# Performance work log

Hardware: AMD Instinct MI355X
Metric: run time of the kernel (lower is better)

## Reference

```python
import jax, jax.numpy as jnp
import numpy as np

B, S, D, H, FF = 2, 2048, 1024, 16, 4096
DH = D // H
EPS = 1e-5


def _linear_params(key, din, dout):
    kw, kb = jax.random.split(key)
    lim = 1.0 / np.sqrt(din)
    W = jax.random.uniform(kw, (din, dout), jnp.float32, -lim, lim)
    b = jax.random.uniform(kb, (dout,), jnp.float32, -lim, lim)
    return W, b


def setup_inputs() -> dict:
    key = jax.random.key(0)
    ks = jax.random.split(key, 8)
    x = jax.random.normal(ks[0], (B, S, D), jnp.float32)
    mask = jnp.ones((B, 1, 1, S), jnp.int32)
    wq, bq = _linear_params(ks[1], D, D)
    wk, bk = _linear_params(ks[2], D, D)
    wv, bv = _linear_params(ks[3], D, D)
    w1, b1 = _linear_params(ks[4], D, D)       # linear1 (attn output proj)
    fw1, fb1 = _linear_params(ks[5], D, FF)    # ffn.w_1
    fw2, fb2 = _linear_params(ks[6], FF, D)    # ffn.w_2
    g1 = jnp.ones((D,), jnp.float32); be1 = jnp.zeros((D,), jnp.float32)
    g2 = jnp.ones((D,), jnp.float32); be2 = jnp.zeros((D,), jnp.float32)
    return dict(x=x, mask=mask, wq=wq, bq=bq, wk=wk, bk=bk, wv=wv, bv=bv,
                w1=w1, b1=b1, g1=g1, be1=be1,
                fw1=fw1, fb1=fb1, fw2=fw2, fb2=fb2, g2=g2, be2=be2)


def _layernorm(x, g, b):
    mu = jnp.mean(x, axis=-1, keepdims=True)
    var = jnp.mean(jnp.square(x - mu), axis=-1, keepdims=True)
    return (x - mu) * jax.lax.rsqrt(var + EPS) * g + b


def _encoder(x, mask, wq, bq, wk, bk, wv, bv, w1, b1, g1, be1,
             fw1, fb1, fw2, fb2, g2, be2):
    res = x
    # QKV projections, reshape to [B, H, S, DH]
    q = (x @ wq + bq).reshape(B, S, H, DH).transpose(0, 2, 1, 3)
    k = (x @ wk + bk).reshape(B, S, H, DH).transpose(0, 2, 1, 3)
    v = (x @ wv + bv).reshape(B, S, H, DH).transpose(0, 2, 1, 3)
    scores = jnp.einsum('bhqd,bhkd->bhqk', q, k) / np.sqrt(DH).astype(np.float32)
    scores = jnp.where(mask == 0, jnp.float32(-1e9), scores)
    probs = jax.nn.softmax(scores, axis=-1)  # dropout = identity in eval
    attn = jnp.einsum('bhqk,bhkd->bhqd', probs, v)
    attn = attn.transpose(0, 2, 1, 3).reshape(B, S, D)
    x = _layernorm(attn @ w1 + b1 + res, g1, be1)
    res = x
    ff = jax.nn.relu(x @ fw1 + fb1) @ fw2 + fb2
    return _layernorm(ff + res, g2, be2)


def reference(x, mask, wq, bq, wk, bk, wv, bv, w1, b1, g1, be1,
              fw1, fb1, fw2, fb2, g2, be2):
    return _encoder(x, mask, wq, bq, wk, bk, wv, bv, w1, b1, g1, be1,
                    fw1, fb1, fw2, fb2, g2, be2)
```

## Files before the change

kernel.cpp:

```cpp
#include <hip/hip_runtime.h>
#include <hip/hip_bf16.h>
#include <cstdint>

typedef unsigned short u16;
typedef __attribute__((ext_vector_type(8))) short bf16x8;
typedef __attribute__((ext_vector_type(4))) float f32x4;

#define DEVFN static __device__ __forceinline__

static constexpr int S    = 2048;
static constexpr int D    = 1024;
static constexpr int DHd  = 64;
static constexpr int FFd  = 4096;
static constexpr int M    = 4096;
static constexpr int LDQK = 2048;

static constexpr float SC2 = 0.18033688f;

DEVFN u16 f2b(float v) {
    union { __hip_bfloat16 h; u16 u; } x;
    x.h = __float2bfloat16(v);
    return x.u;
}
DEVFN float b2f(u16 u) {
    union { float f; uint32_t i; } x;
    x.i = ((uint32_t)u) << 16;
    return x.f;
}

typedef const uint32_t __attribute__((address_space(1)))* gptr_t;
typedef uint32_t __attribute__((address_space(3)))* lptr_t;
DEVFN void load16(const void* g, void* l) {
    __builtin_amdgcn_global_load_lds((gptr_t)g, (lptr_t)l, 16, 0, 0);
}

template<int MODE, int KS>
__global__ __launch_bounds__(512, 2)
void gemm256(const u16* __restrict__ A, const u16* __restrict__ BT,
             const float* __restrict__ bias, void* __restrict__ outp,
             u16* __restrict__ vout, int N)
{
    __shared__ __align__(16) u16 Lds[65536];
    const int tid  = threadIdx.x;
    const int lane = tid & 63;
    const int w    = tid >> 6;
    const int wm = w >> 2, wn = w & 3;
    const int g = lane >> 4, c = lane & 15;
    const int c7 = c & 7;
    const int bn0 = blockIdx.x * 256;
    const int bm0 = blockIdx.y * 256;
    const int z   = (MODE == 4) ? (int)blockIdx.z : 0;
    const size_t kofs = (size_t)z * 1024;

    const int sr = tid >> 3;
    const int gl = (tid & 7) ^ (sr & 7);
    const u16* Asrc = A  + (size_t)(bm0 + sr) * KS + kofs + gl * 8;
    const u16* Bsrc = BT + (size_t)(bn0 + sr) * KS + kofs + gl * 8;
    char* dA = (char*)Lds + (size_t)tid * 16;
    char* dB = dA + 32768;

#define STG_A(BUF, H, KT)                                                       \
    { _Pragma("unroll") for (int Lh = 0; Lh < 2; ++Lh)                          \
        load16(Asrc + (size_t)((H)*128 + Lh*64) * KS + (KT)*64,                 \
               dA + (BUF)*65536 + (H)*16384 + Lh*8192); }
#define STG_B(BUF, H, KT)                                                       \
    { _Pragma("unroll") for (int Lh = 0; Lh < 2; ++Lh)                          \
        load16(Bsrc + (size_t)((H)*128 + Lh*64) * KS + (KT)*64,                 \
               dB + (BUF)*65536 + (H)*16384 + Lh*8192); }
#define VMCNT(N_) asm volatile("s_waitcnt vmcnt(" #N_ ")" ::: "memory")
#define BAR() { __builtin_amdgcn_s_barrier(); __builtin_amdgcn_sched_barrier(0); }

    const char* lbase = (const char*)Lds;
    auto rdA = [&](int buf, int i, int kk) -> bf16x8 {
        const int half = i >> 2;
        const int lr = (2*(i & 3) + wm) * 16 + c;
        return *(const bf16x8*)(lbase + buf*65536 + half*16384 + lr*128
                                + (((kk<<2) + g) ^ c7) * 16);
    };
    auto rdB = [&](int buf, int j, int kk) -> bf16x8 {
        const int half = j >> 1;
        const int lr = (j & 1)*64 + wn*16 + c;
        return *(const bf16x8*)(lbase + buf*65536 + 32768 + half*16384 + lr*128
                                + (((kk<<2) + g) ^ c7) * 16);
    };

    const f32x4 fz = {0.f, 0.f, 0.f, 0.f};
    f32x4 acc[8][4];
#pragma unroll
    for (int i = 0; i < 8; ++i)
#pragma unroll
        for (int j = 0; j < 4; ++j) acc[i][j] = fz;

    bf16x8 af[4][2], bf[4][2];

    auto body = [&](int cur, int nxt, int kt, bool stage) {
        if (stage) STG_A(nxt, 0, kt + 1);
#pragma unroll
        for (int i = 0; i < 4; ++i)
#pragma unroll
            for (int kk = 0; kk < 2; ++kk) af[i][kk] = rdA(cur, i, kk);
#pragma unroll
        for (int j = 0; j < 2; ++j)
#pragma unroll
            for (int kk = 0; kk < 2; ++kk) bf[j][kk] = rdB(cur, j, kk);
        __builtin_amdgcn_s_setprio(1);
#pragma unroll
        for (int i = 0; i < 4; ++i)
#pragma unroll
            for (int j = 0; j < 2; ++j)
#pragma unroll
                for (int kk = 0; kk < 2; ++kk)
                    acc[i][j] = __builtin_amdgcn_mfma_f32_16x16x32_bf16(
                        af[i][kk], bf[j][kk], acc[i][j], 0, 0, 0);
        __builtin_amdgcn_s_setprio(0);
        if (stage) { VMCNT(4); } else { VMCNT(2); }
        BAR();
        if (stage) STG_B(nxt, 0, kt + 1);
#pragma unroll
        for (int j = 2; j < 4; ++j)
#pragma unroll
            for (int kk = 0; kk < 2; ++kk) bf[j][kk] = rdB(cur, j, kk);
        __builtin_amdgcn_s_setprio(1);
#pragma unroll
        for (int i = 0; i < 4; ++i)
#pragma unroll
            for (int j = 2; j < 4; ++j)
#pragma unroll
                for (int kk = 0; kk < 2; ++kk)
                    acc[i][j] = __builtin_amdgcn_mfma_f32_16x16x32_bf16(
                        af[i][kk], bf[j][kk], acc[i][j], 0, 0, 0);
        __builtin_amdgcn_s_setprio(0);
        if (stage) { VMCNT(4); } else { VMCNT(0); }
        BAR();
        if (stage) STG_B(nxt, 1, kt + 1);
#pragma unroll
        for (int i = 4; i < 8; ++i)
#pragma unroll
            for (int kk = 0; kk < 2; ++kk) af[i - 4][kk] = rdA(cur, i, kk);
        __builtin_amdgcn_s_setprio(1);
#pragma unroll
        for (int i = 4; i < 8; ++i)
#pragma unroll
            for (int j = 0; j < 2; ++j)
#pragma unroll
                for (int kk = 0; kk < 2; ++kk)
                    acc[i][j] = __builtin_amdgcn_mfma_f32_16x16x32_bf16(
                        af[i - 4][kk], bf[j][kk], acc[i][j], 0, 0, 0);
        __builtin_amdgcn_s_setprio(0);
        if (stage) STG_A(nxt, 1, kt + 1);
        __builtin_amdgcn_s_setprio(1);
#pragma unroll
        for (int i = 4; i < 8; ++i)
#pragma unroll
            for (int j = 2; j < 4; ++j)
#pragma unroll
                for (int kk = 0; kk < 2; ++kk)
                    acc[i][j] = __builtin_amdgcn_mfma_f32_16x16x32_bf16(
                        af[i - 4][kk], bf[j][kk], acc[i][j], 0, 0, 0);
        __builtin_amdgcn_s_setprio(0);
        if (stage) { VMCNT(4); BAR(); }
    };

    STG_A(0, 0, 0); STG_B(0, 0, 0); STG_B(0, 1, 0); STG_A(0, 1, 0);
    VMCNT(4);
    BAR();

#pragma unroll 1
    for (int kt = 0; kt < 14; kt += 2) {
        body(0, 1, kt, true);
        body(1, 0, kt + 1, true);
    }
    body(0, 1, 14, true);
    body(1, 0, 15, false);
#undef STG_A
#undef STG_B
#undef VMCNT
#undef BAR

#pragma unroll
    for (int i = 0; i < 8; ++i) {
        const int fm = (i >> 2) * 8 + (i & 3) * 2 + wm;
        const int row = bm0 + fm * 16 + 4 * g;
#pragma unroll
        for (int j = 0; j < 4; ++j) {
            const int fn = (j >> 1) * 8 + (j & 1) * 4 + wn;
            const int col = bn0 + fn * 16 + c;
            if (MODE == 4) {
                u16* outz = (u16*)outp + (size_t)z * M * D;
#pragma unroll
                for (int r = 0; r < 4; ++r)
                    outz[(size_t)(row + r) * D + col] = f2b(acc[i][j][r]);
            } else if (MODE == 3 && col >= 2048) {
                const float bv = bias[col];
                union { u16 u[4]; uint2 v; } pk;
#pragma unroll
                for (int r = 0; r < 4; ++r) pk.u[r] = f2b(acc[i][j][r] + bv);
                const size_t vidx = ((size_t)(row >> 11) * 1024 + (col - 2048))
                                    * (size_t)S + (row & 2047);
                *(uint2*)&vout[vidx] = pk.v;
            } else {
                const float bv = bias[col];
                const float sc = (MODE == 3 && col < D) ? SC2 : 1.f;
                const int nn = (MODE == 3) ? LDQK : N;
#pragma unroll
                for (int r = 0; r < 4; ++r) {
                    float v = acc[i][j][r] + bv;
                    if (MODE == 2) v = v > 0.f ? v : 0.f;
                    v *= sc;
                    ((u16*)outp)[(size_t)(row + r) * nn + col] = f2b(v);
                }
            }
        }
    }
}

template<int KTOT>
__global__ __launch_bounds__(256, 3)
void gemm_splitk(const u16* __restrict__ A, const u16* __restrict__ BT,
                 u16* __restrict__ part)
{
    __shared__ __align__(16) u16 As[128 * 64];
    __shared__ __align__(16) u16 Bs[128 * 64];
    const int tid  = threadIdx.x;
    const int lane = tid & 63;
    const int w    = tid >> 6;
    const int wm = w >> 1, wn = w & 1;
    const int g = lane >> 4, c = lane & 15;
    const int bn0 = blockIdx.x * 128;
    const int bm0 = blockIdx.y * 128;
    const int z   = blockIdx.z;
    const int srow = tid >> 3;
    const int scol = (tid & 7) * 8;

    const f32x4 fz = {0.f, 0.f, 0.f, 0.f};
    f32x4 acc[4][4];
#pragma unroll
    for (int i = 0; i < 4; ++i)
#pragma unroll
        for (int j = 0; j < 4; ++j) acc[i][j] = fz;

    const u16* Ab = A  + (size_t)(bm0 + srow) * KTOT + z * (KTOT/2) + scol;
    const u16* Bb = BT + (size_t)(bn0 + srow) * KTOT + z * (KTOT/2) + scol;
    char* AsB = (char*)As + (size_t)tid * 16;
    char* BsB = (char*)Bs + (size_t)tid * 16;

    for (int kt = 0; kt < KTOT/128; ++kt) {
        const int k0 = kt << 6;
        __syncthreads();
#pragma unroll
        for (int cc = 0; cc < 4; ++cc) {
            load16(Ab + (size_t)(cc * 32) * KTOT + k0, AsB + cc * 4096);
            load16(Bb + (size_t)(cc * 32) * KTOT + k0, BsB + cc * 4096);
        }
        __syncthreads();
#pragma unroll
        for (int kk = 0; kk < 2; ++kk) {
            bf16x8 af[4], bfv[4];
#pragma unroll
            for (int i = 0; i < 4; ++i)
                af[i] = *(const bf16x8*)&As[(wm*64 + i*16 + c) * 64 + kk*32 + g*8];
#pragma unroll
            for (int j = 0; j < 4; ++j)
                bfv[j] = *(const bf16x8*)&Bs[(wn*64 + j*16 + c) * 64 + kk*32 + g*8];
#pragma unroll
            for (int i = 0; i < 4; ++i)
#pragma unroll
                for (int j = 0; j < 4; ++j)
                    acc[i][j] = __builtin_amdgcn_mfma_f32_16x16x32_bf16(
                        af[i], bfv[j], acc[i][j], 0, 0, 0);
        }
    }

    u16* outz = part + (size_t)z * M * D;
#pragma unroll
    for (int i = 0; i < 4; ++i) {
        const int row = bm0 + wm*64 + i*16 + g*4;
#pragma unroll
        for (int j = 0; j < 4; ++j) {
            const int col = bn0 + wn*64 + j*16 + c;
#pragma unroll
            for (int r = 0; r < 4; ++r)
                outz[(size_t)(row + r) * D + col] = f2b(acc[i][j][r]);
        }
    }
}

template<int NPART>
__global__ __launch_bounds__(256)
void ln_part_fused(const u16* __restrict__ part, const float* __restrict__ bias,
                   const float* __restrict__ resid, const float* __restrict__ gam,
                   const float* __restrict__ bet, u16* __restrict__ out_b,
                   float* __restrict__ out_f)
{
    const int row = blockIdx.x;
    const int tid = threadIdx.x;
    __shared__ float red1[4], red2[4];
    const float4 bv = ((const float4*)bias)[tid];
    const float4 rv = ((const float4*)(resid + (size_t)row * D))[tid];
    float y0 = bv.x + rv.x, y1 = bv.y + rv.y, y2 = bv.z + rv.z, y3 = bv.w + rv.w;
#pragma unroll
    for (int p = 0; p < NPART; ++p) {
        union { u16 u[4]; uint2 v; } pk;
        pk.v = *(const uint2*)&part[(size_t)(p * M + row) * D + tid * 4];
        y0 += b2f(pk.u[0]); y1 += b2f(pk.u[1]);
        y2 += b2f(pk.u[2]); y3 += b2f(pk.u[3]);
    }
    float s1 = y0 + y1 + y2 + y3;
#pragma unroll
    for (int off = 1; off < 64; off <<= 1) s1 += __shfl_xor(s1, off);
    if ((tid & 63) == 0) red1[tid >> 6] = s1;
    __syncthreads();
    const float mu = (red1[0] + red1[1] + red1[2] + red1[3]) * (1.f / 1024.f);
    const float d0 = y0 - mu, d1 = y1 - mu, d2 = y2 - mu, d3 = y3 - mu;
    float s2 = d0*d0 + d1*d1 + d2*d2 + d3*d3;
#pragma unroll
    for (int off = 1; off < 64; off <<= 1) s2 += __shfl_xor(s2, off);
    if ((tid & 63) == 0) red2[tid >> 6] = s2;
    __syncthreads();
    const float var = (red2[0] + red2[1] + red2[2] + red2[3]) * (1.f / 1024.f);
    const float rs = rsqrtf(var + 1e-5f);
    const int c0 = tid * 4;
    const float o0 = d0 * rs * gam[c0+0] + bet[c0+0];
    const float o1 = d1 * rs * gam[c0+1] + bet[c0+1];
    const float o2 = d2 * rs * gam[c0+2] + bet[c0+2];
    const float o3 = d3 * rs * gam[c0+3] + bet[c0+3];
    if (out_b) {
        union { u16 u[4]; uint2 v; } pk;
        pk.u[0] = f2b(o0); pk.u[1] = f2b(o1); pk.u[2] = f2b(o2); pk.u[3] = f2b(o3);
        ((uint2*)(out_b + (size_t)row * D))[tid] = pk.v;
    }
    if (out_f) {
        float4 yv; yv.x = o0; yv.y = o1; yv.z = o2; yv.w = o3;
        ((float4*)(out_f + (size_t)row * D))[tid] = yv;
    }
}

__global__ __launch_bounds__(256, 3)
void attn_fwd10(const u16* __restrict__ QK, const u16* __restrict__ VT,
                u16* __restrict__ Ob)
{
    __shared__ __align__(16) u16 Ks[3][64 * 64];
    __shared__ __align__(16) u16 Vs[3][64 * 64];
    __shared__ __align__(16) u16 Ps[4][32 * 72];
    const int tid  = threadIdx.x;
    const int lane = tid & 63;
    const int w    = tid >> 6;
    const int g = lane >> 4, c = lane & 15;

    int wid = (int)blockIdx.y * 16 + (int)blockIdx.x;
    wid = (wid & 7) * 64 + (wid >> 3);
    const int bh = wid >> 4;
    const int b = bh >> 4, h = bh & 15;
    const int q0 = (wid & 15) * 128 + w * 32;

    const u16* Qb = QK;
    const u16* Kb = QK + 1024;

    bf16x8 aq[2][2];
#pragma unroll
    for (int rt = 0; rt < 2; ++rt)
#pragma unroll
        for (int kk = 0; kk < 2; ++kk)
            aq[rt][kk] = *(const bf16x8*)&Qb[(size_t)(b*S + q0 + rt*16 + c) * LDQK
                                             + h*DHd + kk*32 + g*8];

    const f32x4 fz = {0.f, 0.f, 0.f, 0.f};
    const short one_b = (short)0x3F80;
    const bf16x8 onesv = {one_b, one_b, one_b, one_b, one_b, one_b, one_b, one_b};
    f32x4 o[2][4];
    f32x4 ol[2];
#pragma unroll
    for (int rt = 0; rt < 2; ++rt) {
        ol[rt] = fz;
#pragma unroll
        for (int j = 0; j < 4; ++j) o[rt][j] = fz;
    }

    const int sr = tid >> 3;
    const int glog = (tid & 7) ^ (sr & 7);
    const u16* Ksrc = Kb + (size_t)(b*S + sr) * LDQK + h*DHd + glog*8;
    const u16* Vsrc = VT + (size_t)(bh*DHd + sr) * S + glog*8;
    char* Kd0 = (char*)&Ks[0][0] + (size_t)tid * 16;
    char* Vd0 = (char*)&Vs[0][0] + (size_t)tid * 16;

#define STAGE(BUFI, kt_)                                                        \
    {                                                                           \
        const int kr0_ = (kt_) * 64;                                            \
        _Pragma("unroll")                                                       \
        for (int cc = 0; cc < 2; ++cc) {                                        \
            load16(Ksrc + (size_t)(kr0_ + cc*32) * LDQK, Kd0 + (BUFI)*8192 + cc*4096); \
            load16(Vsrc + (size_t)(cc*32) * S + kr0_,    Vd0 + (BUFI)*8192 + cc*4096); \
        }                                                                       \
    }
#define WAITBAR(N)                                                              \
    {                                                                           \
        asm volatile("s_waitcnt vmcnt(" #N ")" ::: "memory");                   \
        __builtin_amdgcn_s_barrier();                                           \
        __builtin_amdgcn_sched_barrier(0);                                      \
    }

    u16* pw = &Ps[w][0];
    const int c7 = c & 7;

    auto tile_body = [&](const u16* K0, const u16* V0) {
        bf16x8 bk[4][2];
#pragma unroll
        for (int j = 0; j < 4; ++j)
#pragma unroll
            for (int kk = 0; kk < 2; ++kk)
                bk[j][kk] = *(const bf16x8*)&K0[(j*16 + c) * 64 + (((kk<<2)+g) ^ c7) * 8];

#pragma unroll
        for (int rt = 0; rt < 2; ++rt) {
            f32x4 sv[4];
            __builtin_amdgcn_s_setprio(1);
#pragma unroll
            for (int j = 0; j < 4; ++j) {
                sv[j] = fz;
#pragma unroll
                for (int kk = 0; kk < 2; ++kk)
                    sv[j] = __builtin_amdgcn_mfma_f32_16x16x32_bf16(
                        bk[j][kk], aq[rt][kk], sv[j], 0, 0, 0);
            }
            __builtin_amdgcn_s_setprio(0);

#pragma unroll
            for (int j = 0; j < 4; ++j) {
                const float p0 = exp2f(sv[j][0]);
                const float p1 = exp2f(sv[j][1]);
                const float p2 = exp2f(sv[j][2]);
                const float p3 = exp2f(sv[j][3]);
                union { u16 u[4]; uint2 v; } pk;
                pk.u[0] = f2b(p0); pk.u[1] = f2b(p1);
                pk.u[2] = f2b(p2); pk.u[3] = f2b(p3);
                *(uint2*)&pw[(rt*16 + c) * 72 + j*16 + g*4] = pk.v;
            }
        }

        __builtin_amdgcn_s_setprio(1);
#pragma unroll
        for (int st = 0; st < 2; ++st) {
            bf16x8 bv[4];
#pragma unroll
            for (int j = 0; j < 4; ++j)
                bv[j] = *(const bf16x8*)&V0[(j*16 + c) * 64 + (((st<<2)+g) ^ c7) * 8];
#pragma unroll
            for (int rt = 0; rt < 2; ++rt) {
                const bf16x8 ap = *(const bf16x8*)&pw[(rt*16 + c) * 72 + st*32 + g*8];
#pragma unroll
                for (int j = 0; j < 4; ++j)
                    o[rt][j] = __builtin_amdgcn_mfma_f32_16x16x32_bf16(
                        ap, bv[j], o[rt][j], 0, 0, 0);
                ol[rt] = __builtin_amdgcn_mfma_f32_16x16x32_bf16(
                    ap, onesv, ol[rt], 0, 0, 0);
            }
        }
        __builtin_amdgcn_s_setprio(0);
    };

    STAGE(0, 0);
    STAGE(1, 1);
    WAITBAR(4);

    int kt = 0;
#pragma unroll 1
    for (int it = 0; it < 10; ++it, kt += 3) {
        STAGE(2, kt + 2); tile_body(&Ks[0][0], &Vs[0][0]); WAITBAR(4);
        STAGE(0, kt + 3); tile_body(&Ks[1][0], &Vs[1][0]); WAITBAR(4);
        STAGE(1, kt + 4); tile_body(&Ks[2][0], &Vs[2][0]); WAITBAR(4);
    }
    tile_body(&Ks[0][0], &Vs[0][0]); WAITBAR(0);
    tile_body(&Ks[1][0], &Vs[1][0]);
#undef STAGE
#undef WAITBAR

#pragma unroll
    for (int rt = 0; rt < 2; ++rt) {
#pragma unroll
        for (int r = 0; r < 4; ++r) {
            const float rl = __builtin_amdgcn_rcpf(ol[rt][r]);
            const size_t row = (size_t)(b*S + q0 + rt*16 + 4*g + r) * D + h*DHd;
#pragma unroll
            for (int j = 0; j < 4; ++j)
                Ob[row + j*16 + c] = f2b(o[rt][j][r] * rl);
        }
    }
}

__global__ void cast_bf16_k(const float* __restrict__ in, u16* __restrict__ out) {
    const int i = blockIdx.x * blockDim.x + threadIdx.x;
    const float4 v = ((const float4*)in)[i];
    union { u16 u[4]; uint2 p; } pk;
    pk.u[0] = f2b(v.x); pk.u[1] = f2b(v.y); pk.u[2] = f2b(v.z); pk.u[3] = f2b(v.w);
    ((uint2*)out)[i] = pk.p;
}

__global__ void concat3_k(const float* __restrict__ a, const float* __restrict__ b,
                          const float* __restrict__ c, float* __restrict__ o) {
    const int i = blockIdx.x * blockDim.x + threadIdx.x;
    o[i] = i < 1024 ? a[i] : (i < 2048 ? b[i - 1024] : c[i - 2048]);
}

__global__ __launch_bounds__(256)
void transpose_all_k(const float* __restrict__ wq, const float* __restrict__ wk,
                     const float* __restrict__ wv, const float* __restrict__ w1,
                     const float* __restrict__ fw1, const float* __restrict__ fw2,
                     u16* __restrict__ WqkvT, u16* __restrict__ W1T,
                     u16* __restrict__ F1T, u16* __restrict__ F2T)
{
    __shared__ float tile[32][33];
    const int blk = blockIdx.x;
    const float* src; u16* dst; int R, C, c0, r0;
    if (blk < 3072) {
        const int z = blk >> 10, t = blk & 1023;
        src = z == 0 ? wq : (z == 1 ? wk : wv);
        dst = WqkvT + (size_t)z * D * D;
        R = D; C = D; c0 = (t & 31) * 32; r0 = (t >> 5) * 32;
    } else if (blk < 4096) {
        const int t = blk - 3072;
        src = w1; dst = W1T;
        R = D; C = D; c0 = (t & 31) * 32; r0 = (t >> 5) * 32;
    } else if (blk < 8192) {
        const int t = blk - 4096;
        src = fw1; dst = F1T;
        R = D; C = FFd; c0 = (t & 127) * 32; r0 = (t >> 7) * 32;
    } else {
        const int t = blk - 8192;
        src = fw2; dst = F2T;
        R = FFd; C = D; c0 = (t & 31) * 32; r0 = (t >> 5) * 32;
    }
    const int tx = threadIdx.x & 31, ty = threadIdx.x >> 5;
#pragma unroll
    for (int i = 0; i < 4; ++i)
        tile[ty + i*8][tx] = src[(size_t)(r0 + ty + i*8) * C + c0 + tx];
    __syncthreads();
#pragma unroll
    for (int i = 0; i < 4; ++i)
        dst[(size_t)(c0 + ty + i*8) * R + r0 + tx] = f2b(tile[tx][ty + i*8]);
}

extern "C" void kernel_launch(void* const* d_in, const int* in_sizes, int n_in,
                              void* d_out, int out_size, void* d_ws, size_t ws_size,
                              hipStream_t stream)
{
    (void)in_sizes; (void)n_in; (void)out_size; (void)ws_size;
    const float* x   = (const float*)d_in[0];
    const float* wq  = (const float*)d_in[2];
    const float* bq  = (const float*)d_in[3];
    const float* wk  = (const float*)d_in[4];
    const float* bk  = (const float*)d_in[5];
    const float* wv  = (const float*)d_in[6];
    const float* bv  = (const float*)d_in[7];
    const float* w1  = (const float*)d_in[8];
    const float* b1  = (const float*)d_in[9];
    const float* g1  = (const float*)d_in[10];
    const float* be1 = (const float*)d_in[11];
    const float* fw1 = (const float*)d_in[12];
    const float* fb1 = (const float*)d_in[13];
    const float* fw2 = (const float*)d_in[14];
    const float* fb2 = (const float*)d_in[15];
    const float* g2  = (const float*)d_in[16];
    const float* be2 = (const float*)d_in[17];

    char* ws = (char*)d_ws;
    size_t off = 0;
    auto alloc = [&](size_t bytes) -> void* {
        void* p = ws + off;
        off += (bytes + 255) & ~(size_t)255;
        return p;
    };
    u16*   QKb   = (u16*)alloc((size_t)M * LDQK * 2);
    u16*   VTh   = (u16*)alloc((size_t)M * D * 2);
    u16*   Ob    = (u16*)alloc((size_t)M * D * 2);
    u16*   Xb    = (u16*)alloc((size_t)M * D * 2);
    u16*   WqkvT = (u16*)alloc((size_t)3 * D * D * 2);
    u16*   W1T   = (u16*)alloc((size_t)D * D * 2);
    u16*   F1T   = (u16*)alloc((size_t)D * FFd * 2);
    u16*   F2T   = (u16*)alloc((size_t)D * FFd * 2);
    float* x1f   = (float*)alloc((size_t)M * D * 4);
    u16*   x1b   = (u16*)alloc((size_t)M * D * 2);
    u16*   Hb    = (u16*)alloc((size_t)M * FFd * 2);
    float* bqkv  = (float*)alloc((size_t)3 * D * 4);

    u16* Part = QKb;

    cast_bf16_k<<<dim3(M * D / 1024), dim3(256), 0, stream>>>(x, Xb);
    transpose_all_k<<<dim3(12288), dim3(256), 0, stream>>>(
        wq, wk, wv, w1, fw1, fw2, WqkvT, W1T, F1T, F2T);
    concat3_k<<<dim3(3 * D / 256), dim3(256), 0, stream>>>(bq, bk, bv, bqkv);

    gemm256<3, D><<<dim3(3 * D / 256, M/256), 512, 0, stream>>>(
        Xb, WqkvT, bqkv, QKb, VTh, LDQK);

    attn_fwd10<<<dim3(S/128, 32), 256, 0, stream>>>(QKb, VTh, Ob);

    gemm_splitk<D><<<dim3(D/128, M/128, 2), 256, 0, stream>>>(Ob, W1T, Part);

    ln_part_fused<2><<<dim3(M), 256, 0, stream>>>(Part, b1, x, g1, be1, x1b, x1f);

    gemm256<2, D><<<dim3(FFd/256, M/256), 512, 0, stream>>>(
        x1b, F1T, fb1, Hb, nullptr, FFd);

    gemm256<4, FFd><<<dim3(D/256, M/256, 4), 512, 0, stream>>>(
        Hb, F2T, nullptr, Part, nullptr, D);

    ln_part_fused<4><<<dim3(M), 256, 0, stream>>>(Part, fb2, x1f, g2, be2,
                                                  nullptr, (float*)d_out);
}
```

Measured before the change: 226.5 us.

## Split attention over KV halves with merge, fuse prep kernels, use bf16 residual

Attention is split into two halves over the key dimension, doubling the block count to 1024. Each block writes unnormalized partial outputs and row sums, and a new merge kernel adds and normalizes them. The KV pipeline drops from triple to double buffering. The cast, transpose and bias-concat prep kernels become one launch, and the second layernorm reads the bf16 copy of x1 as its residual instead of an fp32 copy. These trade an extra merge pass, and lower residual precision, for more parallelism and fewer launches.

```diff
diff --git a/kernel.cpp b/kernel.cpp
--- a/kernel.cpp
+++ b/kernel.cpp
@@ -285,19 +285,27 @@
     }
 }
 
-template<int NPART>
+template<int NPART, bool BRES>
 __global__ __launch_bounds__(256)
 void ln_part_fused(const u16* __restrict__ part, const float* __restrict__ bias,
-                   const float* __restrict__ resid, const float* __restrict__ gam,
-                   const float* __restrict__ bet, u16* __restrict__ out_b,
-                   float* __restrict__ out_f)
+                   const float* __restrict__ residf, const u16* __restrict__ residb,
+                   const float* __restrict__ gam, const float* __restrict__ bet,
+                   u16* __restrict__ out_b, float* __restrict__ out_f)
 {
     const int row = blockIdx.x;
     const int tid = threadIdx.x;
     __shared__ float red1[4], red2[4];
     const float4 bv = ((const float4*)bias)[tid];
-    const float4 rv = ((const float4*)(resid + (size_t)row * D))[tid];
-    float y0 = bv.x + rv.x, y1 = bv.y + rv.y, y2 = bv.z + rv.z, y3 = bv.w + rv.w;
+    float y0 = bv.x, y1 = bv.y, y2 = bv.z, y3 = bv.w;
+    if (BRES) {
+        union { u16 u[4]; uint2 v; } rk;
+        rk.v = *(const uint2*)&residb[(size_t)row * D + tid * 4];
+        y0 += b2f(rk.u[0]); y1 += b2f(rk.u[1]);
+        y2 += b2f(rk.u[2]); y3 += b2f(rk.u[3]);
+    } else {
+        const float4 rv = ((const float4*)(residf + (size_t)row * D))[tid];
+        y0 += rv.x; y1 += rv.y; y2 += rv.z; y3 += rv.w;
+    }
 #pragma unroll
     for (int p = 0; p < NPART; ++p) {
         union { u16 u[4]; uint2 v; } pk;
@@ -336,22 +344,25 @@
 }
 
 __global__ __launch_bounds__(256, 3)
-void attn_fwd10(const u16* __restrict__ QK, const u16* __restrict__ VT,
-                u16* __restrict__ Ob)
+void attn_fwd11(const u16* __restrict__ QK, const u16* __restrict__ VT,
+                u16* __restrict__ Op, float* __restrict__ Lp)
 {
-    __shared__ __align__(16) u16 Ks[3][64 * 64];
-    __shared__ __align__(16) u16 Vs[3][64 * 64];
+    __shared__ __align__(16) u16 Ks[2][64 * 64];
+    __shared__ __align__(16) u16 Vs[2][64 * 64];
     __shared__ __align__(16) u16 Ps[4][32 * 72];
     const int tid  = threadIdx.x;
     const int lane = tid & 63;
     const int w    = tid >> 6;
     const int g = lane >> 4, c = lane & 15;
 
-    int wid = (int)blockIdx.y * 16 + (int)blockIdx.x;
-    wid = (wid & 7) * 64 + (wid >> 3);
-    const int bh = wid >> 4;
+    int wid = (int)blockIdx.x;
+    wid = (wid & 7) * 128 + (wid >> 3);
+    const int bh   = wid >> 5;
+    const int half = (wid >> 4) & 1;
+    const int qt   = wid & 15;
     const int b = bh >> 4, h = bh & 15;
-    const int q0 = (wid & 15) * 128 + w * 32;
+    const int q0 = qt * 128 + w * 32;
+    const int kt0 = half * 16;
 
     const u16* Qb = QK;
     const u16* Kb = QK + 1024;
@@ -458,58 +469,81 @@
         __builtin_amdgcn_s_setprio(0);
     };
 
-    STAGE(0, 0);
-    STAGE(1, 1);
-    WAITBAR(4);
-
-    int kt = 0;
+    STAGE(0, kt0);
+    WAITBAR(0);
 #pragma unroll 1
-    for (int it = 0; it < 10; ++it, kt += 3) {
-        STAGE(2, kt + 2); tile_body(&Ks[0][0], &Vs[0][0]); WAITBAR(4);
-        STAGE(0, kt + 3); tile_body(&Ks[1][0], &Vs[1][0]); WAITBAR(4);
-        STAGE(1, kt + 4); tile_body(&Ks[2][0], &Vs[2][0]); WAITBAR(4);
-    }
-    tile_body(&Ks[0][0], &Vs[0][0]); WAITBAR(0);
+    for (int it = 0; it < 7; ++it) {
+        STAGE(1, kt0 + 2*it + 1); tile_body(&Ks[0][0], &Vs[0][0]); WAITBAR(0);
+        STAGE(0, kt0 + 2*it + 2); tile_body(&Ks[1][0], &Vs[1][0]); WAITBAR(0);
+    }
+    STAGE(1, kt0 + 15); tile_body(&Ks[0][0], &Vs[0][0]); WAITBAR(0);
     tile_body(&Ks[1][0], &Vs[1][0]);
 #undef STAGE
 #undef WAITBAR
 
+    u16* Oz = Op + (size_t)half * M * D;
+    float* Lz = Lp + (size_t)(half * 16 + h) * M;
 #pragma unroll
     for (int rt = 0; rt < 2; ++rt) {
 #pragma unroll
         for (int r = 0; r < 4; ++r) {
-            const float rl = __builtin_amdgcn_rcpf(ol[rt][r]);
-            const size_t row = (size_t)(b*S + q0 + rt*16 + 4*g + r) * D + h*DHd;
+            const int grow = b*S + q0 + rt*16 + 4*g + r;
+            if (c == 0) Lz[grow] = ol[rt][r];
+            const size_t rowo = (size_t)grow * D + h*DHd;
 #pragma unroll
             for (int j = 0; j < 4; ++j)
-                Ob[row + j*16 + c] = f2b(o[rt][j][r] * rl);
+                Oz[rowo + j*16 + c] = f2b(o[rt][j][r]);
         }
     }
 }
 
-__global__ void cast_bf16_k(const float* __restrict__ in, u16* __restrict__ out) {
-    const int i = blockIdx.x * blockDim.x + threadIdx.x;
-    const float4 v = ((const float4*)in)[i];
-    union { u16 u[4]; uint2 p; } pk;
-    pk.u[0] = f2b(v.x); pk.u[1] = f2b(v.y); pk.u[2] = f2b(v.z); pk.u[3] = f2b(v.w);
-    ((uint2*)out)[i] = pk.p;
-}
-
-__global__ void concat3_k(const float* __restrict__ a, const float* __restrict__ b,
-                          const float* __restrict__ c, float* __restrict__ o) {
-    const int i = blockIdx.x * blockDim.x + threadIdx.x;
-    o[i] = i < 1024 ? a[i] : (i < 2048 ? b[i - 1024] : c[i - 2048]);
-}
-
 __global__ __launch_bounds__(256)
-void transpose_all_k(const float* __restrict__ wq, const float* __restrict__ wk,
-                     const float* __restrict__ wv, const float* __restrict__ w1,
-                     const float* __restrict__ fw1, const float* __restrict__ fw2,
-                     u16* __restrict__ WqkvT, u16* __restrict__ W1T,
-                     u16* __restrict__ F1T, u16* __restrict__ F2T)
+void attn_merge(const u16* __restrict__ Op, const float* __restrict__ Lp,
+                u16* __restrict__ Ob)
+{
+    const int idx = blockIdx.x * 256 + threadIdx.x;
+    const int m   = idx >> 7;
+    const int col = (idx & 127) * 8;
+    const int h   = col >> 6;
+    const float rl = __builtin_amdgcn_rcpf(Lp[(size_t)h*M + m] +
+                                           Lp[(size_t)(16+h)*M + m]);
+    union { u16 u[8]; uint4 v; } pa, pb, po;
+    pa.v = *(const uint4*)&Op[(size_t)m*D + col];
+    pb.v = *(const uint4*)&Op[(size_t)(M + m)*D + col];
+#pragma unroll
+    for (int r = 0; r < 8; ++r)
+        po.u[r] = f2b((b2f(pa.u[r]) + b2f(pb.u[r])) * rl);
+    *(uint4*)&Ob[(size_t)m*D + col] = po.v;
+}
+
+__global__ __launch_bounds__(256)
+void prep_all_k(const float* __restrict__ x,
+                const float* __restrict__ wq, const float* __restrict__ wk,
+                const float* __restrict__ wv, const float* __restrict__ w1,
+                const float* __restrict__ fw1, const float* __restrict__ fw2,
+                const float* __restrict__ bq, const float* __restrict__ bk,
+                const float* __restrict__ bv, u16* __restrict__ Xb,
+                u16* __restrict__ WqkvT, u16* __restrict__ W1T,
+                u16* __restrict__ F1T, u16* __restrict__ F2T,
+                float* __restrict__ bqkv)
 {
     __shared__ float tile[32][33];
-    const int blk = blockIdx.x;
+    int blk = blockIdx.x;
+    if (blk < 4096) {
+        const int i = blk * 256 + threadIdx.x;
+        const float4 v = ((const float4*)x)[i];
+        union { u16 u[4]; uint2 p; } pk;
+        pk.u[0] = f2b(v.x); pk.u[1] = f2b(v.y);
+        pk.u[2] = f2b(v.z); pk.u[3] = f2b(v.w);
+        ((uint2*)Xb)[i] = pk.p;
+        return;
+    }
+    blk -= 4096;
+    if (blk >= 12288) {
+        const int i = (blk - 12288) * 256 + threadIdx.x;
+        bqkv[i] = i < 1024 ? bq[i] : (i < 2048 ? bk[i - 1024] : bv[i - 2048]);
+        return;
+    }
     const float* src; u16* dst; int R, C, c0, r0;
     if (blk < 3072) {
         const int z = blk >> 10, t = blk & 1023;
@@ -577,26 +611,28 @@
     u16*   W1T   = (u16*)alloc((size_t)D * D * 2);
     u16*   F1T   = (u16*)alloc((size_t)D * FFd * 2);
     u16*   F2T   = (u16*)alloc((size_t)D * FFd * 2);
-    float* x1f   = (float*)alloc((size_t)M * D * 4);
     u16*   x1b   = (u16*)alloc((size_t)M * D * 2);
     u16*   Hb    = (u16*)alloc((size_t)M * FFd * 2);
     float* bqkv  = (float*)alloc((size_t)3 * D * 4);
 
-    u16* Part = QKb;
-
-    cast_bf16_k<<<dim3(M * D / 1024), dim3(256), 0, stream>>>(x, Xb);
-    transpose_all_k<<<dim3(12288), dim3(256), 0, stream>>>(
-        wq, wk, wv, w1, fw1, fw2, WqkvT, W1T, F1T, F2T);
-    concat3_k<<<dim3(3 * D / 256), dim3(256), 0, stream>>>(bq, bk, bv, bqkv);
+    u16*   Part = QKb;
+    u16*   Opart = Hb;
+    float* Lpart = (float*)(Hb + (size_t)2 * M * D);
+
+    prep_all_k<<<dim3(16396), dim3(256), 0, stream>>>(
+        x, wq, wk, wv, w1, fw1, fw2, bq, bk, bv,
+        Xb, WqkvT, W1T, F1T, F2T, bqkv);
 
     gemm256<3, D><<<dim3(3 * D / 256, M/256), 512, 0, stream>>>(
         Xb, WqkvT, bqkv, QKb, VTh, LDQK);
 
-    attn_fwd10<<<dim3(S/128, 32), 256, 0, stream>>>(QKb, VTh, Ob);
+    attn_fwd11<<<dim3(1024), 256, 0, stream>>>(QKb, VTh, Opart, Lpart);
+    attn_merge<<<dim3(2048), 256, 0, stream>>>(Opart, Lpart, Ob);
 
     gemm_splitk<D><<<dim3(D/128, M/128, 2), 256, 0, stream>>>(Ob, W1T, Part);
 
-    ln_part_fused<2><<<dim3(M), 256, 0, stream>>>(Part, b1, x, g1, be1, x1b, x1f);
+    ln_part_fused<2, false><<<dim3(M), 256, 0, stream>>>(
+        Part, b1, x, nullptr, g1, be1, x1b, nullptr);
 
     gemm256<2, D><<<dim3(FFd/256, M/256), 512, 0, stream>>>(
         x1b, F1T, fb1, Hb, nullptr, FFd);
@@ -604,6 +640,6 @@
     gemm256<4, FFd><<<dim3(D/256, M/256, 4), 512, 0, stream>>>(
         Hb, F2T, nullptr, Part, nullptr, D);
 
-    ln_part_fused<4><<<dim3(M), 256, 0, stream>>>(Part, fb2, x1f, g2, be2,
-                                                  nullptr, (float*)d_out);
-}
+    ln_part_fused<4, true><<<dim3(M), 256, 0, stream>>>(
+        Part, fb2, nullptr, x1b, g2, be2, nullptr, (float*)d_out);
+}
```

Result: faster. 221.1 us (median of 2 runs) (-2.4%).
